# Performance work log

Measured on AMD Instinct MI355X. Metric: run time of the kernel, lower is better.

The kernel has to match this reference:

```python
import jax, jax.numpy as jnp
import numpy as np

B, S, C = 64, 1024, 512
EPS = 1e-5

def setup_inputs() -> dict:
    key = jax.random.key(0)
    k1, k2, k3 = jax.random.split(key, 3)
    x = jax.random.normal(k1, (B, S, C), dtype=jnp.float32)
    # LayerNorm affine over normalized_shape=[S, C]
    ln_w = jnp.ones((S, C), dtype=jnp.float32)
    ln_b = jnp.zeros((S, C), dtype=jnp.float32)
    # Linear(seq_len, seq_len): torch init U(-1/sqrt(S), 1/sqrt(S))
    bound = 1.0 / np.sqrt(S)
    lin_w = jax.random.uniform(k2, (S, S), jnp.float32, -bound, bound)
    lin_b = jax.random.uniform(k3, (S,), jnp.float32, -bound, bound)
    return {"x": x, "ln_w": ln_w, "ln_b": ln_b, "lin_w": lin_w, "lin_b": lin_b}

def reference(x, ln_w, ln_b, lin_w, lin_b):
    # LayerNorm over last two dims [S, C]
    mu = jnp.mean(x, axis=(1, 2), keepdims=True)
    var = jnp.mean(jnp.square(x - mu), axis=(1, 2), keepdims=True)
    h = (x - mu) * jax.lax.rsqrt(var + EPS) * ln_w + ln_b
    # permute -> [B, C, S], linear over S, relu, permute back, residual
    # fused as einsum over the seq axis directly (no explicit transpose)
    y = jnp.einsum('bsc,ts->btc', h, lin_w) + lin_b[None, :, None]
    y = jax.nn.relu(y)
    return x + y
```

## Files before the change

kernel.cpp:

```cpp
#include <hip/hip_runtime.h>
#include <stdint.h>

#define BB 64
#define SS 1024
#define CC 512
#define EPS 1e-5f

typedef __attribute__((ext_vector_type(8))) __bf16 bf16x8;
typedef __attribute__((ext_vector_type(8))) unsigned short ushort8v;
typedef __attribute__((ext_vector_type(4))) float f32x4;

__device__ __forceinline__ unsigned short f2bf(float f) {
    unsigned int u = __builtin_bit_cast(unsigned int, f);
    u += 0x7fffu + ((u >> 16) & 1u);
    return (unsigned short)(u >> 16);
}
__device__ __forceinline__ float bf2f(unsigned short u) {
    return __builtin_bit_cast(float, (uint32_t)u << 16);
}

__global__ __launch_bounds__(256) void k_prep(const float* __restrict__ x,
                                              const float* __restrict__ lnw,
                                              const float* __restrict__ lnb,
                                              const float* __restrict__ linw,
                                              unsigned short* __restrict__ Wb,
                                              unsigned short* __restrict__ Ht,
                                              float* __restrict__ psum,
                                              float* __restrict__ psq) {
    const int id = blockIdx.x;
    const int t = threadIdx.x;
    if (id >= 8448) {
        int i = (id - 8448) * 256 + t;
        float4 v = ((const float4*)linw)[i];
        ushort4 o;
        o.x = f2bf(v.x); o.y = f2bf(v.y); o.z = f2bf(v.z); o.w = f2bf(v.w);
        ((ushort4*)Wb)[i] = o;
        return;
    }
    __shared__ uint32_t lds[64 * 33];
    __shared__ float ls[4], lq[4];
    int b, rem;
    const float* src;
    const float* wp;
    if (id < 8192)      { b = id >> 7; rem = id & 127; src = x + (size_t)b * SS * CC; wp = lnw; }
    else if (id < 8320) { b = 64; rem = id - 8192; src = lnw; wp = nullptr; }
    else                { b = 65; rem = id - 8320; src = lnb; wp = nullptr; }
    const int s0 = (rem >> 3) << 6;
    const int c0 = (rem & 7) << 6;
    const int cq = t & 15, spA = t >> 4;
    float sA = 0.f, qA = 0.f;
#pragma unroll
    for (int h = 0; h < 2; ++h) {
        int sp = spA + h * 16;
        int sl = s0 + 2 * sp;
        int cc = c0 + 4 * cq;
        size_t xb = (size_t)sl * CC + cc;
        float4 a0 = *(const float4*)(src + xb);
        float4 a1 = *(const float4*)(src + xb + CC);
        float4 g0 = a0, g1 = a1;
        if (wp) {
            float4 w0 = *(const float4*)(wp + xb);
            float4 w1 = *(const float4*)(wp + xb + CC);
            g0.x = a0.x * w0.x; g0.y = a0.y * w0.y; g0.z = a0.z * w0.z; g0.w = a0.w * w0.w;
            g1.x = a1.x * w1.x; g1.y = a1.y * w1.y; g1.z = a1.z * w1.z; g1.w = a1.w * w1.w;
            sA += a0.x + a0.y + a0.z + a0.w + a1.x + a1.y + a1.z + a1.w;
            qA += a0.x*a0.x + a0.y*a0.y + a0.z*a0.z + a0.w*a0.w
                + a1.x*a1.x + a1.y*a1.y + a1.z*a1.z + a1.w*a1.w;
        }
        uint32_t u0 = (uint32_t)f2bf(g0.x) | ((uint32_t)f2bf(g1.x) << 16);
        uint32_t u1 = (uint32_t)f2bf(g0.y) | ((uint32_t)f2bf(g1.y) << 16);
        uint32_t u2 = (uint32_t)f2bf(g0.z) | ((uint32_t)f2bf(g1.z) << 16);
        uint32_t u3 = (uint32_t)f2bf(g0.w) | ((uint32_t)f2bf(g1.w) << 16);
        lds[(4 * cq + 0) * 33 + sp] = u0;
        lds[(4 * cq + 1) * 33 + sp] = u1;
        lds[(4 * cq + 2) * 33 + sp] = u2;
        lds[(4 * cq + 3) * 33 + sp] = u3;
    }
    if (wp) {
        for (int off = 32; off; off >>= 1) {
            sA += __shfl_down(sA, off, 64);
            qA += __shfl_down(qA, off, 64);
        }
        if ((t & 63) == 0) { ls[t >> 6] = sA; lq[t >> 6] = qA; }
    }
    __syncthreads();
    int spq = t & 7, clA = t >> 3;
#pragma unroll
    for (int h = 0; h < 2; ++h) {
        int cl = clA + h * 32;
        uint4 v;
        v.x = lds[cl * 33 + spq * 4 + 0];
        v.y = lds[cl * 33 + spq * 4 + 1];
        v.z = lds[cl * 33 + spq * 4 + 2];
        v.w = lds[cl * 33 + spq * 4 + 3];
        size_t o = (((size_t)b * CC + c0 + cl) * SS + (size_t)s0 + spq * 8) >> 3;
        ((uint4*)Ht)[o] = v;
    }
    if (wp && t == 0) {
        psum[id] = ls[0] + ls[1] + ls[2] + ls[3];
        psq[id]  = lq[0] + lq[1] + lq[2] + lq[3];
    }
}

__global__ __launch_bounds__(128) void k_stats2(const float* __restrict__ psum,
                                                const float* __restrict__ psq,
                                                float* __restrict__ mu,
                                                float* __restrict__ rsg) {
    int b = blockIdx.x, t = threadIdx.x;
    float s = psum[b * 128 + t];
    float q = psq[b * 128 + t];
    for (int off = 32; off; off >>= 1) {
        s += __shfl_down(s, off, 64);
        q += __shfl_down(q, off, 64);
    }
    __shared__ float ls[2], lq[2];
    if ((t & 63) == 0) { ls[t >> 6] = s; lq[t >> 6] = q; }
    __syncthreads();
    if (t == 0) {
        float ss = ls[0] + ls[1], qq = lq[0] + lq[1];
        const float inv = 1.f / (float)(SS * CC);
        float m = ss * inv;
        float v = qq * inv - m * m;
        mu[b] = m;
        rsg[b] = rsqrtf(v + EPS);
    }
}

template<bool FINAL>
__global__ __launch_bounds__(256) void k_gemm(const unsigned short* __restrict__ A,
                                              const unsigned short* __restrict__ Htall,
                                              const float* __restrict__ x,
                                              const float* __restrict__ linb,
                                              const unsigned short* __restrict__ wlb,
                                              const unsigned short* __restrict__ blb,
                                              const float* __restrict__ muA,
                                              const float* __restrict__ rsA,
                                              float* __restrict__ out) {
    int b, tm, tn;
    if constexpr (FINAL) {
        int xcd = blockIdx.x & 7;
        int local = blockIdx.x >> 3;
        b = xcd * 8 + (local >> 5);
        tn = (local >> 3) & 3;
        tm = local & 7;
    } else {
        tn = blockIdx.x; tm = blockIdx.y; b = 64 + blockIdx.z;
    }
    __shared__ __align__(16) unsigned short SM[24576];
    const int tid = threadIdx.x;
    const int lane = tid & 63;
    const int w = tid >> 6;
    const int wm = w >> 1, wn = w & 1;
    const int quad = lane >> 4, l15 = lane & 15;

    f32x4 acc[4][4];
#pragma unroll
    for (int mi = 0; mi < 4; ++mi)
#pragma unroll
        for (int ni = 0; ni < 4; ++ni)
            acc[mi][ni] = (f32x4){0.f, 0.f, 0.f, 0.f};

    const unsigned short* Ab = A + (size_t)(tm * 128) * 1024;
    const unsigned short* Bb = Htall + ((size_t)b * 512 + tn * 128) * 1024;
    const int srow = tid >> 2;
    const int scol = ((tid & 3) ^ ((srow >> 1) & 3)) * 8;

    auto stage = [&](int buf, int k0) {
#pragma unroll
        for (int q = 0; q < 2; ++q) {
            __builtin_amdgcn_global_load_lds(
                (const __attribute__((address_space(1))) void*)(Ab + (size_t)(q * 64 + srow) * 1024 + k0 + scol),
                (__attribute__((address_space(3))) void*)(SM + buf * 8192 + q * 2048 + w * 512),
                16, 0, 0);
            __builtin_amdgcn_global_load_lds(
                (const __attribute__((address_space(1))) void*)(Bb + (size_t)(q * 64 + srow) * 1024 + k0 + scol),
                (__attribute__((address_space(3))) void*)(SM + buf * 8192 + 4096 + q * 2048 + w * 512),
                16, 0, 0);
        }
    };
    const int fs = (l15 >> 1) & 3;
    auto compute = [&](int buf) {
        const unsigned short* as = SM + buf * 8192;
        const unsigned short* bs = SM + buf * 8192 + 4096;
        bf16x8 av[4], bv[4];
#pragma unroll
        for (int i = 0; i < 4; ++i) {
            ushort8v a  = *(const ushort8v*)&as[(wm * 64 + i * 16 + l15) * 32 + (quad ^ fs) * 8];
            ushort8v b2 = *(const ushort8v*)&bs[(wn * 64 + i * 16 + l15) * 32 + (quad ^ fs) * 8];
            av[i] = __builtin_bit_cast(bf16x8, a);
            bv[i] = __builtin_bit_cast(bf16x8, b2);
        }
#pragma unroll
        for (int mi = 0; mi < 4; ++mi)
#pragma unroll
            for (int ni = 0; ni < 4; ++ni)
                acc[mi][ni] = __builtin_amdgcn_mfma_f32_16x16x32_bf16(
                    av[mi], bv[ni], acc[mi][ni], 0, 0, 0);
    };

    stage(0, 0);
    stage(1, 32);
    for (int j = 0; j < 31; ++j) {
        asm volatile("s_waitcnt vmcnt(4)" ::: "memory");
        __builtin_amdgcn_sched_barrier(0);
        __builtin_amdgcn_s_barrier();
        __builtin_amdgcn_sched_barrier(0);
        int k2 = (j + 2) * 32;
        if (k2 < 1024) stage((j + 2) % 3, k2);
        compute(j % 3);
    }
    asm volatile("s_waitcnt vmcnt(0)" ::: "memory");
    __builtin_amdgcn_sched_barrier(0);
    __builtin_amdgcn_s_barrier();
    __builtin_amdgcn_sched_barrier(0);
    compute(31 % 3);

    if constexpr (FINAL) {
        __syncthreads();
        const float rsv  = rsA[b];
        const float rsmu = rsv * muA[b];
        float* eps = (float*)SM + (w << 11);
#pragma unroll
        for (int ch = 0; ch < 2; ++ch) {
#pragma unroll
            for (int m2 = 0; m2 < 2; ++m2) {
                int mi = ch * 2 + m2;
#pragma unroll
                for (int ni = 0; ni < 4; ++ni)
#pragma unroll
                    for (int r = 0; r < 4; ++r)
                        eps[(m2 * 16 + quad * 4 + r) * 64 + ni * 16 + l15] = acc[mi][ni][r];
            }
#pragma unroll
            for (int jj = 0; jj < 8; ++jj) {
                int row = jj * 4 + quad;
                int tt = tm * 128 + wm * 64 + ch * 32 + row;
                int cc = tn * 128 + wn * 64 + l15 * 4;
                size_t o2 = (size_t)tt * 512 + cc;
                size_t o  = ((size_t)b * 1024 + tt) * 512 + cc;
                f32x4 v    = *(f32x4*)&eps[row * 64 + l15 * 4];
                ushort4 wv4 = *(const ushort4*)&wlb[o2];
                ushort4 bv4 = *(const ushort4*)&blb[o2];
                f32x4 xv   = *(const f32x4*)&x[o];
                float we[4] = {bf2f(wv4.x), bf2f(wv4.y), bf2f(wv4.z), bf2f(wv4.w)};
                float be[4] = {bf2f(bv4.x), bf2f(bv4.y), bf2f(bv4.z), bf2f(bv4.w)};
                f32x4 ov;
#pragma unroll
                for (int e = 0; e < 4; ++e) {
                    float vv = rsv * v[e] - rsmu * we[e] + be[e];
                    vv = vv > 0.f ? vv : 0.f;
                    ov[e] = xv[e] + vv;
                }
                *(f32x4*)&out[o] = ov;
            }
        }
    } else {
        int z = b - 64;
        unsigned short* o16 = (unsigned short*)out;
#pragma unroll
        for (int mi = 0; mi < 4; ++mi) {
#pragma unroll
            for (int r = 0; r < 4; ++r) {
                int tt = tm * 128 + wm * 64 + mi * 16 + quad * 4 + r;
                float add = z ? linb[tt] : 0.f;
#pragma unroll
                for (int ni = 0; ni < 4; ++ni) {
                    int cc = tn * 128 + wn * 64 + ni * 16 + l15;
                    o16[((size_t)z * 1024 + tt) * 512 + cc] = f2bf(acc[mi][ni][r] + add);
                }
            }
        }
    }
}

extern "C" void kernel_launch(void* const* d_in, const int* in_sizes, int n_in,
                              void* d_out, int out_size, void* d_ws, size_t ws_size,
                              hipStream_t stream) {
    (void)in_sizes; (void)n_in; (void)out_size; (void)ws_size;
    const float* x    = (const float*)d_in[0];
    const float* lnw  = (const float*)d_in[1];
    const float* lnb  = (const float*)d_in[2];
    const float* linw = (const float*)d_in[3];
    const float* linb = (const float*)d_in[4];
    float* out = (float*)d_out;

    char* ws = (char*)d_ws;
    unsigned short* Wb  = (unsigned short*)ws;
    unsigned short* Ht  = (unsigned short*)(ws + (2u << 20));
    unsigned short* wlb = (unsigned short*)(ws + (68u << 20));
    unsigned short* blb = wlb + 512 * 1024;
    float* psum = (float*)(ws + (72u << 20));
    float* psq  = psum + 8192;
    float* mu   = psq + 8192;
    float* rsg  = mu + 64;

    k_prep<<<9472, 256, 0, stream>>>(x, lnw, lnb, linw, Wb, Ht, psum, psq);
    k_stats2<<<64, 128, 0, stream>>>(psum, psq, mu, rsg);
    k_gemm<false><<<dim3(4, 8, 2), 256, 0, stream>>>(Wb, Ht, nullptr, linb,
                                                     nullptr, nullptr, nullptr, nullptr,
                                                     (float*)wlb);
    k_gemm<true><<<2048, 256, 0, stream>>>(Wb, Ht, x, nullptr,
                                           wlb, blb, mu, rsg, out);
}
```

Measured before the change: 384.5 us.

## Process two batches per GEMM block to reuse the shared weight tile

After: 364.7 us. -5.1%, faster.

```diff
diff --git a/kernel.cpp b/kernel.cpp
--- a/kernel.cpp
+++ b/kernel.cpp
@@ -127,81 +127,93 @@
 }
 
 template<bool FINAL>
-__global__ __launch_bounds__(256) void k_gemm(const unsigned short* __restrict__ A,
-                                              const unsigned short* __restrict__ Htall,
-                                              const float* __restrict__ x,
-                                              const float* __restrict__ linb,
-                                              const unsigned short* __restrict__ wlb,
-                                              const unsigned short* __restrict__ blb,
-                                              const float* __restrict__ muA,
-                                              const float* __restrict__ rsA,
-                                              float* __restrict__ out) {
-    int b, tm, tn;
+__global__ __launch_bounds__(256, 2) void k_gemm(const unsigned short* __restrict__ A,
+                                                 const unsigned short* __restrict__ Htall,
+                                                 const float* __restrict__ x,
+                                                 const float* __restrict__ linb,
+                                                 const unsigned short* __restrict__ wlb,
+                                                 const unsigned short* __restrict__ blb,
+                                                 const float* __restrict__ muA,
+                                                 const float* __restrict__ rsA,
+                                                 float* __restrict__ out) {
+    int b0, b1, tm, tn;
     if constexpr (FINAL) {
         int xcd = blockIdx.x & 7;
         int local = blockIdx.x >> 3;
-        b = xcd * 8 + (local >> 5);
-        tn = (local >> 3) & 3;
-        tm = local & 7;
+        int p = xcd * 4 + (local >> 5);
+        int rem = local & 31;
+        tn = rem >> 3; tm = rem & 7;
+        b0 = 2 * p; b1 = 2 * p + 1;
     } else {
-        tn = blockIdx.x; tm = blockIdx.y; b = 64 + blockIdx.z;
-    }
-    __shared__ __align__(16) unsigned short SM[24576];
+        tn = blockIdx.x; tm = blockIdx.y; b0 = 64; b1 = 65;
+    }
+    __shared__ __align__(16) unsigned short SM[36864];
     const int tid = threadIdx.x;
     const int lane = tid & 63;
     const int w = tid >> 6;
     const int wm = w >> 1, wn = w & 1;
     const int quad = lane >> 4, l15 = lane & 15;
 
-    f32x4 acc[4][4];
+    f32x4 acc0[4][4], acc1[4][4];
 #pragma unroll
     for (int mi = 0; mi < 4; ++mi)
 #pragma unroll
-        for (int ni = 0; ni < 4; ++ni)
-            acc[mi][ni] = (f32x4){0.f, 0.f, 0.f, 0.f};
-
-    const unsigned short* Ab = A + (size_t)(tm * 128) * 1024;
-    const unsigned short* Bb = Htall + ((size_t)b * 512 + tn * 128) * 1024;
+        for (int ni = 0; ni < 4; ++ni) {
+            acc0[mi][ni] = (f32x4){0.f, 0.f, 0.f, 0.f};
+            acc1[mi][ni] = (f32x4){0.f, 0.f, 0.f, 0.f};
+        }
+
+    const unsigned short* Ab  = A + (size_t)(tm * 128) * 1024;
+    const unsigned short* Bb0 = Htall + ((size_t)b0 * 512 + tn * 128) * 1024;
+    const unsigned short* Bb1 = Htall + ((size_t)b1 * 512 + tn * 128) * 1024;
     const int srow = tid >> 2;
     const int scol = ((tid & 3) ^ ((srow >> 1) & 3)) * 8;
 
     auto stage = [&](int buf, int k0) {
+        unsigned short* base = SM + buf * 12288;
 #pragma unroll
         for (int q = 0; q < 2; ++q) {
+            size_t roff = (size_t)(q * 64 + srow) * 1024 + k0 + scol;
             __builtin_amdgcn_global_load_lds(
-                (const __attribute__((address_space(1))) void*)(Ab + (size_t)(q * 64 + srow) * 1024 + k0 + scol),
-                (__attribute__((address_space(3))) void*)(SM + buf * 8192 + q * 2048 + w * 512),
-                16, 0, 0);
+                (const __attribute__((address_space(1))) void*)(Ab + roff),
+                (__attribute__((address_space(3))) void*)(base + q * 2048 + w * 512), 16, 0, 0);
             __builtin_amdgcn_global_load_lds(
-                (const __attribute__((address_space(1))) void*)(Bb + (size_t)(q * 64 + srow) * 1024 + k0 + scol),
-                (__attribute__((address_space(3))) void*)(SM + buf * 8192 + 4096 + q * 2048 + w * 512),
-                16, 0, 0);
+                (const __attribute__((address_space(1))) void*)(Bb0 + roff),
+                (__attribute__((address_space(3))) void*)(base + 4096 + q * 2048 + w * 512), 16, 0, 0);
+            __builtin_amdgcn_global_load_lds(
+                (const __attribute__((address_space(1))) void*)(Bb1 + roff),
+                (__attribute__((address_space(3))) void*)(base + 8192 + q * 2048 + w * 512), 16, 0, 0);
         }
     };
     const int fs = (l15 >> 1) & 3;
     auto compute = [&](int buf) {
-        const unsigned short* as = SM + buf * 8192;
-        const unsigned short* bs = SM + buf * 8192 + 4096;
-        bf16x8 av[4], bv[4];
+        const unsigned short* as  = SM + buf * 12288;
+        const unsigned short* bs0 = as + 4096;
+        const unsigned short* bs1 = as + 8192;
+        bf16x8 av[4], bv0[4], bv1[4];
 #pragma unroll
         for (int i = 0; i < 4; ++i) {
-            ushort8v a  = *(const ushort8v*)&as[(wm * 64 + i * 16 + l15) * 32 + (quad ^ fs) * 8];
-            ushort8v b2 = *(const ushort8v*)&bs[(wn * 64 + i * 16 + l15) * 32 + (quad ^ fs) * 8];
-            av[i] = __builtin_bit_cast(bf16x8, a);
-            bv[i] = __builtin_bit_cast(bf16x8, b2);
+            int ar = (wm * 64 + i * 16 + l15) * 32 + (quad ^ fs) * 8;
+            int br = (wn * 64 + i * 16 + l15) * 32 + (quad ^ fs) * 8;
+            av[i]  = __builtin_bit_cast(bf16x8, *(const ushort8v*)&as[ar]);
+            bv0[i] = __builtin_bit_cast(bf16x8, *(const ushort8v*)&bs0[br]);
+            bv1[i] = __builtin_bit_cast(bf16x8, *(const ushort8v*)&bs1[br]);
         }
 #pragma unroll
         for (int mi = 0; mi < 4; ++mi)
 #pragma unroll
-            for (int ni = 0; ni < 4; ++ni)
-                acc[mi][ni] = __builtin_amdgcn_mfma_f32_16x16x32_bf16(
-                    av[mi], bv[ni], acc[mi][ni], 0, 0, 0);
+            for (int ni = 0; ni < 4; ++ni) {
+                acc0[mi][ni] = __builtin_amdgcn_mfma_f32_16x16x32_bf16(
+                    av[mi], bv0[ni], acc0[mi][ni], 0, 0, 0);
+                acc1[mi][ni] = __builtin_amdgcn_mfma_f32_16x16x32_bf16(
+                    av[mi], bv1[ni], acc1[mi][ni], 0, 0, 0);
+            }
     };
 
     stage(0, 0);
     stage(1, 32);
     for (int j = 0; j < 31; ++j) {
-        asm volatile("s_waitcnt vmcnt(4)" ::: "memory");
+        asm volatile("s_waitcnt vmcnt(6)" ::: "memory");
         __builtin_amdgcn_sched_barrier(0);
         __builtin_amdgcn_s_barrier();
         __builtin_amdgcn_sched_barrier(0);
@@ -217,56 +229,64 @@
 
     if constexpr (FINAL) {
         __syncthreads();
-        const float rsv  = rsA[b];
-        const float rsmu = rsv * muA[b];
         float* eps = (float*)SM + (w << 11);
 #pragma unroll
-        for (int ch = 0; ch < 2; ++ch) {
-#pragma unroll
-            for (int m2 = 0; m2 < 2; ++m2) {
-                int mi = ch * 2 + m2;
-#pragma unroll
-                for (int ni = 0; ni < 4; ++ni)
-#pragma unroll
-                    for (int r = 0; r < 4; ++r)
-                        eps[(m2 * 16 + quad * 4 + r) * 64 + ni * 16 + l15] = acc[mi][ni][r];
+        for (int bb = 0; bb < 2; ++bb) {
+            const int b = bb ? b1 : b0;
+            const float rsv  = rsA[b];
+            const float rsmu = rsv * muA[b];
+            f32x4 (&ac)[4][4] = bb ? acc1 : acc0;
+#pragma unroll
+            for (int ch = 0; ch < 2; ++ch) {
+#pragma unroll
+                for (int m2 = 0; m2 < 2; ++m2) {
+                    int mi = ch * 2 + m2;
+#pragma unroll
+                    for (int ni = 0; ni < 4; ++ni)
+#pragma unroll
+                        for (int r = 0; r < 4; ++r)
+                            eps[(m2 * 16 + quad * 4 + r) * 64 + ni * 16 + l15] = ac[mi][ni][r];
+                }
+#pragma unroll
+                for (int jj = 0; jj < 8; ++jj) {
+                    int row = jj * 4 + quad;
+                    int tt = tm * 128 + wm * 64 + ch * 32 + row;
+                    int cc = tn * 128 + wn * 64 + l15 * 4;
+                    size_t o2 = (size_t)tt * 512 + cc;
+                    size_t o  = ((size_t)b * 1024 + tt) * 512 + cc;
+                    f32x4 v    = *(f32x4*)&eps[row * 64 + l15 * 4];
+                    ushort4 wv4 = *(const ushort4*)&wlb[o2];
+                    ushort4 bv4 = *(const ushort4*)&blb[o2];
+                    f32x4 xv   = *(const f32x4*)&x[o];
+                    float we[4] = {bf2f(wv4.x), bf2f(wv4.y), bf2f(wv4.z), bf2f(wv4.w)};
+                    float be[4] = {bf2f(bv4.x), bf2f(bv4.y), bf2f(bv4.z), bf2f(bv4.w)};
+                    f32x4 ov;
+#pragma unroll
+                    for (int e = 0; e < 4; ++e) {
+                        float vv = rsv * v[e] - rsmu * we[e] + be[e];
+                        vv = vv > 0.f ? vv : 0.f;
+                        ov[e] = xv[e] + vv;
+                    }
+                    *(f32x4*)&out[o] = ov;
+                }
             }
-#pragma unroll
-            for (int jj = 0; jj < 8; ++jj) {
-                int row = jj * 4 + quad;
-                int tt = tm * 128 + wm * 64 + ch * 32 + row;
-                int cc = tn * 128 + wn * 64 + l15 * 4;
-                size_t o2 = (size_t)tt * 512 + cc;
-                size_t o  = ((size_t)b * 1024 + tt) * 512 + cc;
-                f32x4 v    = *(f32x4*)&eps[row * 64 + l15 * 4];
-                ushort4 wv4 = *(const ushort4*)&wlb[o2];
-                ushort4 bv4 = *(const ushort4*)&blb[o2];
-                f32x4 xv   = *(const f32x4*)&x[o];
-                float we[4] = {bf2f(wv4.x), bf2f(wv4.y), bf2f(wv4.z), bf2f(wv4.w)};
-                float be[4] = {bf2f(bv4.x), bf2f(bv4.y), bf2f(bv4.z), bf2f(bv4.w)};
-                f32x4 ov;
-#pragma unroll
-                for (int e = 0; e < 4; ++e) {
-                    float vv = rsv * v[e] - rsmu * we[e] + be[e];
-                    vv = vv > 0.f ? vv : 0.f;
-                    ov[e] = xv[e] + vv;
-                }
-                *(f32x4*)&out[o] = ov;
-            }
         }
     } else {
-        int z = b - 64;
         unsigned short* o16 = (unsigned short*)out;
 #pragma unroll
-        for (int mi = 0; mi < 4; ++mi) {
-#pragma unroll
-            for (int r = 0; r < 4; ++r) {
-                int tt = tm * 128 + wm * 64 + mi * 16 + quad * 4 + r;
-                float add = z ? linb[tt] : 0.f;
-#pragma unroll
-                for (int ni = 0; ni < 4; ++ni) {
-                    int cc = tn * 128 + wn * 64 + ni * 16 + l15;
-                    o16[((size_t)z * 1024 + tt) * 512 + cc] = f2bf(acc[mi][ni][r] + add);
+        for (int bb = 0; bb < 2; ++bb) {
+            f32x4 (&ac)[4][4] = bb ? acc1 : acc0;
+#pragma unroll
+            for (int mi = 0; mi < 4; ++mi) {
+#pragma unroll
+                for (int r = 0; r < 4; ++r) {
+                    int tt = tm * 128 + wm * 64 + mi * 16 + quad * 4 + r;
+                    float add = bb ? linb[tt] : 0.f;
+#pragma unroll
+                    for (int ni = 0; ni < 4; ++ni) {
+                        int cc = tn * 128 + wn * 64 + ni * 16 + l15;
+                        o16[((size_t)bb * 1024 + tt) * 512 + cc] = f2bf(ac[mi][ni][r] + add);
+                    }
                 }
             }
         }
@@ -296,9 +316,9 @@
 
     k_prep<<<9472, 256, 0, stream>>>(x, lnw, lnb, linw, Wb, Ht, psum, psq);
     k_stats2<<<64, 128, 0, stream>>>(psum, psq, mu, rsg);
-    k_gemm<false><<<dim3(4, 8, 2), 256, 0, stream>>>(Wb, Ht, nullptr, linb,
-                                                     nullptr, nullptr, nullptr, nullptr,
-                                                     (float*)wlb);
-    k_gemm<true><<<2048, 256, 0, stream>>>(Wb, Ht, x, nullptr,
+    k_gemm<false><<<dim3(4, 8), 256, 0, stream>>>(Wb, Ht, nullptr, linb,
+                                                  nullptr, nullptr, nullptr, nullptr,
+                                                  (float*)wlb);
+    k_gemm<true><<<1024, 256, 0, stream>>>(Wb, Ht, x, nullptr,
                                            wlb, blb, mu, rsg, out);
 }
```
